# Kernel tuning notes

Hardware: AMD Instinct MI355X
Metric: run time of the kernel (lower is better)

The kernel has to match this reference:

```python
import jax, jax.numpy as jnp
import numpy as np

# dims: 64 graphs x 1024 nodes, 32768 edges/graph, 256 feats, 64 pools/graph
B, NPG, EPG, F, C = 64, 1024, 32768, 256, 64
N, E = B * NPG, B * EPG


def setup_inputs() -> dict:
    key = jax.random.key(0)
    k1, k2, k3, k4, k5 = jax.random.split(key, 5)
    x = jax.random.normal(k1, (N, F), jnp.float32)
    # within-graph edges (block structure, as in real batched graphs)
    src = jax.random.randint(k2, (B, EPG), 0, NPG, dtype=jnp.int32)
    dst = jax.random.randint(k3, (B, EPG), 0, NPG, dtype=jnp.int32)
    off = (jnp.arange(B, dtype=jnp.int32) * NPG)[:, None]
    edge_index = jnp.stack([(src + off).reshape(-1), (dst + off).reshape(-1)], 0)
    edge_weight = jax.random.uniform(k4, (E,), jnp.float32)
    batch = jnp.repeat(jnp.arange(B, dtype=jnp.int32), NPG)
    batch_ptr = jnp.arange(B + 1, dtype=jnp.int32) * NPG
    # pooling_net stand-in: linear d_feat -> num_pools
    W = jax.random.normal(k5, (F, C), jnp.float32) * 0.05
    b = jnp.zeros((C,), jnp.float32)
    return dict(x=x, edge_index=edge_index, edge_weight=edge_weight,
                batch=batch, batch_ptr=batch_ptr, W=W, b=b)


def reference(x, edge_index, edge_weight, batch, batch_ptr, W, b):
    num_batches = batch_ptr.shape[0] - 1
    Cp = W.shape[1]  # num_pools_per_graph
    logits = x @ W + b                       # pooling_net(x, edge_index)
    sm = jax.nn.softmax(logits, axis=-1)     # [N, C]
    c = jnp.argmax(sm, axis=-1)              # hard cluster per node [N]
    p = jnp.take_along_axis(sm, c[:, None], axis=-1)[:, 0]
    # straight-through nonzero value of s (==1.0 in forward value)
    v = 1.0 - jax.lax.stop_gradient(p) + p
    gcl = batch * Cp + c                     # global cluster id [N]
    K = num_batches * Cp
    # out = S^T x  -> segment reduce over nodes by global cluster
    out = jax.ops.segment_sum(v[:, None] * x, gcl, num_segments=K)  # [K, F]
    # out_adj = S^T A S  (block diagonal over graphs): per-edge scatter
    src, dst = edge_index[0], edge_index[1]
    ci, cj = c[src], c[dst]
    gb = batch[src]
    flat = gb * (Cp * Cp) + ci * Cp + cj
    contrib = edge_weight * v[src] * v[dst]
    out_adj = jax.ops.segment_sum(contrib, flat, num_segments=num_batches * Cp * Cp)
    # dense block-diagonal index set (torch returns coalesced nonzeros;
    # jit needs static shapes, so we enumerate all within-graph pool pairs)
    idx = jnp.arange(num_batches * Cp * Cp, dtype=jnp.int32)
    bb, rem = idx // (Cp * Cp), idx % (Cp * Cp)
    out_edge_index = jnp.stack([bb * Cp + rem // Cp, bb * Cp + rem % Cp], 0)
    # link_loss = ||A - S S^T||_F / E  via exact decomposition
    a2 = jnp.sum(edge_weight * edge_weight)
    ap = jnp.sum(jnp.where(gcl[src] == gcl[dst], contrib, 0.0))
    vs2 = jax.ops.segment_sum(v * v, gcl, num_segments=K)
    p2 = jnp.sum(vs2 * vs2)
    link_loss = jnp.sqrt(jnp.maximum(a2 - 2.0 * ap + p2, 0.0)) / edge_index.shape[1]
    batch_out = jnp.repeat(jnp.arange(num_batches, dtype=jnp.int32), Cp)
    batch_ptr_out = jnp.arange(num_batches + 1, dtype=jnp.int32) * Cp
    return (out, out_edge_index, out_adj, link_loss, jnp.float32(0.0),
            batch_out, batch_ptr_out)
```

## Files before the change

kernel.cpp:

```cpp
#include <hip/hip_runtime.h>
#include <cstdint>
#include <cstddef>

typedef __attribute__((ext_vector_type(8))) short short8;
typedef __attribute__((ext_vector_type(4))) float f32x4;

#define GLOAD_LDS16(gsrc, ldst) \
    __builtin_amdgcn_global_load_lds( \
        (const __attribute__((address_space(1))) void*)(gsrc), \
        (__attribute__((address_space(3))) void*)(ldst), 16, 0, 0)

namespace {
constexpr int kN    = 65536;
constexpr int kF    = 256;
constexpr int kC    = 64;
constexpr int kNPG  = 1024;
constexpr int kB    = 64;
constexpr int kE    = 2097152;
constexpr int kK    = kB * kC;

constexpr size_t OFF_OUT  = 0;
constexpr size_t OFF_EIDX = (size_t)kK * kF;
constexpr size_t OFF_ADJ  = OFF_EIDX + 2ull*kB*kC*kC;
constexpr size_t OFF_LL   = OFF_ADJ + (size_t)kB*kC*kC;
constexpr size_t OFF_Z    = OFF_LL + 1;
constexpr size_t OFF_BOUT = OFF_Z + 1;
constexpr size_t OFF_BPTR = OFF_BOUT + kK;

constexpr size_t WS_C    = 0;
constexpr size_t WS_V    = 262144;
constexpr size_t WS_VS2  = 524288;
constexpr size_t WS_A2   = 540672;
constexpr size_t WS_PERM = 544768;
constexpr size_t WS_STRT = 806912;
constexpr size_t WS_WPH  = 1048576;
constexpr size_t WS_WPL  = 1081344;
constexpr size_t WS_PADJ = 544768;

__device__ __forceinline__ unsigned short bf16_rn(float f)
{
    const unsigned int b = __float_as_uint(f);
    return (unsigned short)((b + 0x7fffu + ((b >> 16) & 1u)) >> 16);
}
}

__global__ __launch_bounds__(256) void k_const(float* __restrict__ out,
                                               const float* __restrict__ Wm,
                                               unsigned short* __restrict__ wph,
                                               unsigned short* __restrict__ wpl)
{
    const int i = blockIdx.x * 256 + threadIdx.x;
    constexpr int E2 = 2 * kB * kC * kC;
    constexpr int B3 = E2 + kK + kB + 1;
    if (i < E2) {
        const int half = i >= kB*kC*kC;
        const int idx  = half ? i - kB*kC*kC : i;
        const int bb = idx >> 12, rem = idx & 4095;
        const int val = half ? bb*kC + (rem & 63) : bb*kC + (rem >> 6);
        out[OFF_EIDX + i] = (float)val;
    } else if (i < E2 + kK) {
        const int j = i - E2;
        out[OFF_BOUT + j] = (float)(j >> 6);
    } else if (i < B3) {
        const int j = i - (E2 + kK);
        out[OFF_BPTR + j] = (float)(j * kC);
    } else if (i < B3 + 32768) {
        const int j  = (i - B3) & 16383;
        const int lo = (i - B3) >= 16384;
        const int jj = j & 7, lane = (j >> 3) & 63;
        const int nt = (j >> 9) & 3, ks = j >> 11;
        const float wv = Wm[(size_t)(ks*32 + (lane>>4)*8 + jj)*kC
                            + nt*16 + (lane & 15)];
        const unsigned short h = bf16_rn(wv);
        if (!lo) {
            wph[j] = h;
        } else {
            const float hf = __uint_as_float((unsigned int)h << 16);
            wpl[j] = bf16_rn(wv - hf);
        }
    }
}

__global__ __launch_bounds__(256) void k_logits(
    const float* __restrict__ x, const unsigned short* __restrict__ wph,
    const unsigned short* __restrict__ wpl, const float* __restrict__ bv,
    int* __restrict__ carr, float* __restrict__ varr)
{
    __shared__ unsigned short wlds[32768];
    __shared__ float xsl[2][64 * 32];
    const int tid  = threadIdx.x;
    const int lane = tid & 63;
    const int w    = tid >> 6;
    const int nbase = blockIdx.x * 64;
    const int l15  = lane & 15;
    const int kgrp = lane >> 4;

    const int snode = lane >> 3;
    const int sfo   = ((lane & 7) ^ snode) * 4;

    f32x4 acc[4];
#pragma unroll
    for (int nt = 0; nt < 4; ++nt) acc[nt] = f32x4{0.f, 0.f, 0.f, 0.f};

#pragma unroll
    for (int t = 0; t < 8; ++t) {
        GLOAD_LDS16(wph + ((size_t)t*256 + tid)*8,
                    &wlds[(t*256 + w*64)*8]);
        GLOAD_LDS16(wpl + ((size_t)t*256 + tid)*8,
                    &wlds[16384 + (t*256 + w*64)*8]);
    }
#pragma unroll
    for (int i = 0; i < 2; ++i) {
        const float* src = x + (size_t)(nbase + w*16 + i*8 + snode)*kF + sfo;
        GLOAD_LDS16(src, &xsl[0][(w*16 + i*8)*32]);
    }
    asm volatile("s_waitcnt vmcnt(0)" ::: "memory");
    __syncthreads();

#pragma unroll 1
    for (int c = 0; c < 8; ++c) {
        if (c < 7) {
#pragma unroll
            for (int i = 0; i < 2; ++i) {
                const float* src = x + (size_t)(nbase + w*16 + i*8 + snode)*kF
                                     + (c+1)*32 + sfo;
                GLOAD_LDS16(src, &xsl[(c+1) & 1][(w*16 + i*8)*32]);
            }
            asm volatile("s_waitcnt vmcnt(2)" ::: "memory");
        } else {
            asm volatile("s_waitcnt vmcnt(0)" ::: "memory");
        }

        const float* __restrict__ xb = &xsl[c & 1][0];
        short8 bh[4], bl[4];
#pragma unroll
        for (int nt = 0; nt < 4; ++nt) {
            const int wo = ((c*4 + nt)*64 + lane) * 8;
            bh[nt] = *reinterpret_cast<const short8*>(&wlds[wo]);
            bl[nt] = *reinterpret_cast<const short8*>(&wlds[16384 + wo]);
        }
        const int row = w*16 + l15;
        const int sA  = ((kgrp*2)     ^ (l15 & 7)) * 4;
        const int sC  = ((kgrp*2 + 1) ^ (l15 & 7)) * 4;
        const float4 xa = *reinterpret_cast<const float4*>(&xb[row*32 + sA]);
        const float4 xc = *reinterpret_cast<const float4*>(&xb[row*32 + sC]);
        const float xv[8] = {xa.x, xa.y, xa.z, xa.w,
                             xc.x, xc.y, xc.z, xc.w};
        short8 ah, al;
#pragma unroll
        for (int j = 0; j < 8; ++j) {
            const unsigned short h = bf16_rn(xv[j]);
            const float hf = __uint_as_float((unsigned int)h << 16);
            ah[j] = (short)h;
            al[j] = (short)bf16_rn(xv[j] - hf);
        }
#pragma unroll
        for (int nt = 0; nt < 4; ++nt) {
            acc[nt] = __builtin_amdgcn_mfma_f32_16x16x32_bf16(
                ah, bh[nt], acc[nt], 0, 0, 0);
            acc[nt] = __builtin_amdgcn_mfma_f32_16x16x32_bf16(
                al, bh[nt], acc[nt], 0, 0, 0);
            acc[nt] = __builtin_amdgcn_mfma_f32_16x16x32_bf16(
                ah, bl[nt], acc[nt], 0, 0, 0);
            acc[nt] = __builtin_amdgcn_mfma_f32_16x16x32_bf16(
                al, bl[nt], acc[nt], 0, 0, 0);
        }
    }

#pragma unroll
    for (int nt = 0; nt < 4; ++nt) {
        const float b = bv[nt*16 + l15];
#pragma unroll
        for (int r = 0; r < 4; ++r) acc[nt][r] += b;
    }
#pragma unroll
    for (int r = 0; r < 4; ++r) {
        float m = acc[0][r]; int ci = l15;
#pragma unroll
        for (int nt = 1; nt < 4; ++nt) {
            if (acc[nt][r] > m) { m = acc[nt][r]; ci = nt*16 + l15; }
        }
#pragma unroll
        for (int off = 1; off < 16; off <<= 1) {
            const float om = __shfl_xor(m, off);
            const int   oc = __shfl_xor(ci, off);
            if (om > m || (om == m && oc < ci)) { m = om; ci = oc; }
        }
        float s = 0.f;
#pragma unroll
        for (int nt = 0; nt < 4; ++nt) s += expf(acc[nt][r] - m);
#pragma unroll
        for (int off = 1; off < 16; off <<= 1) s += __shfl_xor(s, off);
        if (l15 == r) {
            const float p = 1.0f / s;
            const int n = nbase + w*16 + kgrp*4 + r;
            carr[n] = ci;
            varr[n] = (1.0f - p) + p;
        }
    }
}

__global__ __launch_bounds__(1024) void k_sort(
    const int* __restrict__ carr, int* __restrict__ perm,
    int* __restrict__ startc)
{
    __shared__ int hist[16][64];
    __shared__ int startS[65];
    const int g = blockIdx.x;
    const int tid = threadIdx.x;
    const int w = tid >> 6, lane = tid & 63;
    const int c = carr[g*kNPG + tid];
    hist[tid >> 6][tid & 63] = 0;
    __syncthreads();
    unsigned long long mm = ~0ull;
#pragma unroll
    for (int b = 0; b < 6; ++b) {
        const unsigned long long bal = __ballot((c >> b) & 1);
        mm &= ((c >> b) & 1) ? bal : ~bal;
    }
    const unsigned long long ltmask =
        (lane == 0) ? 0ull : (~0ull >> (64 - lane));
    const int rank_in_wave = __popcll(mm & ltmask);
    const int leader = __ffsll((unsigned long long)mm) - 1;
    if (lane == leader) hist[w][c] = __popcll(mm);
    __syncthreads();
    if (w == 0) {
        int tot = 0;
#pragma unroll
        for (int i = 0; i < 16; ++i) tot += hist[i][lane];
        int pre = tot;
#pragma unroll
        for (int off = 1; off < 64; off <<= 1) {
            const int t = __shfl_up(pre, off);
            if (lane >= off) pre += t;
        }
        startS[lane + 1] = pre;
        if (lane == 0) startS[0] = 0;
    }
    __syncthreads();
    int before = startS[c];
    for (int i = 0; i < w; ++i) before += hist[i][c];
    perm[g*kNPG + before + rank_in_wave] = g*kNPG + tid;
    if (tid < 65) startc[g*65 + tid] = startS[tid];
}

__global__ __launch_bounds__(1024) void k_pool_x(
    const float* __restrict__ x, const int* __restrict__ perm,
    const int* __restrict__ startc, const float* __restrict__ varr,
    float* __restrict__ out, float* __restrict__ vs2)
{
    const int tid  = threadIdx.x;
    const int g    = blockIdx.x >> 3;
    const int fh   = blockIdx.x & 7;
    const int w    = tid >> 6;
    const int lane = tid & 63;
    const int q    = lane & 7;
    const int sub  = lane >> 3;
    const int fbase = fh*32 + q*4;
#pragma unroll
    for (int cc = 0; cc < 4; ++cc) {
        const int c = w*4 + cc;
        const int s = startc[g*65 + c];
        const int e = startc[g*65 + c + 1];
        float ax = 0.f, ay = 0.f, az = 0.f, aw = 0.f, v2 = 0.f;
        for (int base = s + sub; base < e; base += 8) {
            const int n = perm[(size_t)g*kNPG + base];
            const float v = varr[n];
            const float4 xv = *reinterpret_cast<const float4*>(
                x + (size_t)n*kF + fbase);
            ax = fmaf(v, xv.x, ax); ay = fmaf(v, xv.y, ay);
            az = fmaf(v, xv.z, az); aw = fmaf(v, xv.w, aw);
            v2 = fmaf(v, v, v2);
        }
#pragma unroll
        for (int off = 8; off < 64; off <<= 1) {
            ax += __shfl_xor(ax, off); ay += __shfl_xor(ay, off);
            az += __shfl_xor(az, off); aw += __shfl_xor(aw, off);
            v2 += __shfl_xor(v2, off);
        }
        if (sub == 0) {
            const float4 o = {ax, ay, az, aw};
            *reinterpret_cast<float4*>(
                out + OFF_OUT + (size_t)(g*kC + c)*kF + fbase) = o;
        }
        if (fh == 0 && lane == 0) vs2[g*kC + c] = v2;
    }
}

__global__ __launch_bounds__(1024) void k_adj(
    const int* __restrict__ ei, const float* __restrict__ ew,
    const int* __restrict__ carr, const float* __restrict__ varr,
    float* __restrict__ padj, float* __restrict__ a2p)
{
    __shared__ float adj[kC*kC];
    __shared__ float vls[kNPG];
    __shared__ int   cls[kNPG];
    __shared__ float wred[16];
    const int tid = threadIdx.x;
    const int bid = blockIdx.x;
    const int g   = bid >> 3;
    for (int i = tid; i < kC*kC; i += 1024) adj[i] = 0.f;
    vls[tid] = varr[g*kNPG + tid];
    cls[tid] = carr[g*kNPG + tid];
    __syncthreads();
    const int e0 = bid * 4096;
    float a2l = 0.f;
#pragma unroll
    for (int it = 0; it < 4; ++it) {
        const int e  = e0 + it*1024 + tid;
        const int sn = ei[e]      & (kNPG - 1);
        const int dn = ei[kE + e] & (kNPG - 1);
        const float wv = ew[e];
        a2l += wv * wv;
        atomicAdd(&adj[cls[sn]*kC + cls[dn]], wv * vls[sn] * vls[dn]);
    }
    __syncthreads();
#pragma unroll
    for (int r = 0; r < 4; ++r) {
        const int lin = r*1024 + tid;
        padj[(size_t)bid*4096 + lin] = adj[lin];
    }
#pragma unroll
    for (int off = 32; off > 0; off >>= 1) a2l += __shfl_down(a2l, off);
    if ((tid & 63) == 0) wred[tid >> 6] = a2l;
    __syncthreads();
    if (tid == 0) {
        float s = 0.f;
#pragma unroll
        for (int wv = 0; wv < 16; ++wv) s += wred[wv];
        a2p[bid] = s;
    }
}

__global__ __launch_bounds__(256) void k_adj_merge(
    const float* __restrict__ padj, float* __restrict__ out)
{
    const int id = blockIdx.x*256 + threadIdx.x;
    const int g = id >> 12, idx = id & 4095;
    float s = 0.f;
#pragma unroll
    for (int sp = 0; sp < 8; ++sp) s += padj[(size_t)(g*8 + sp)*4096 + idx];
    out[OFF_ADJ + id] = s;
}

__global__ __launch_bounds__(256) void k_final(
    const float* __restrict__ vs2, const float* __restrict__ a2p,
    float* __restrict__ out)
{
    const int tid = threadIdx.x;
    float p2l = 0.f, apl = 0.f;
#pragma unroll
    for (int r = 0; r < 16; ++r) {
        const int k = r*256 + tid;
        const float t = vs2[k];
        p2l += t*t;
        const int g = k >> 6, cc = k & 63;
        apl += out[OFF_ADJ + (size_t)g*4096 + cc*65];
    }
    float a2l = a2p[tid] + a2p[tid + 256];
#pragma unroll
    for (int off = 32; off > 0; off >>= 1) {
        p2l += __shfl_down(p2l, off);
        apl += __shfl_down(apl, off);
        a2l += __shfl_down(a2l, off);
    }
    __shared__ float red[3][4];
    if ((tid & 63) == 0) {
        red[0][tid>>6] = p2l; red[1][tid>>6] = apl; red[2][tid>>6] = a2l;
    }
    __syncthreads();
    if (tid == 0) {
        const float p2 = red[0][0]+red[0][1]+red[0][2]+red[0][3];
        const float ap = red[1][0]+red[1][1]+red[1][2]+red[1][3];
        const float a2 = red[2][0]+red[2][1]+red[2][2]+red[2][3];
        const float val = a2 - 2.0f*ap + p2;
        out[OFF_LL] = sqrtf(fmaxf(val, 0.f)) / (float)kE;
        out[OFF_Z]  = 0.0f;
    }
}

extern "C" void kernel_launch(void* const* d_in, const int* in_sizes, int n_in,
                              void* d_out, int out_size, void* d_ws, size_t ws_size,
                              hipStream_t stream)
{
    const float* x  = (const float*)d_in[0];
    const int*   ei = (const int*)d_in[1];
    const float* ew = (const float*)d_in[2];
    const float* Wm = (const float*)d_in[5];
    const float* bv = (const float*)d_in[6];
    float* out = (float*)d_out;
    char*  ws  = (char*)d_ws;
    int*   carr  = (int*)(ws + WS_C);
    float* varr  = (float*)(ws + WS_V);
    float* vs2   = (float*)(ws + WS_VS2);
    float* a2p   = (float*)(ws + WS_A2);
    int*   perm  = (int*)(ws + WS_PERM);
    int*   strt  = (int*)(ws + WS_STRT);
    unsigned short* wph = (unsigned short*)(ws + WS_WPH);
    unsigned short* wpl = (unsigned short*)(ws + WS_WPL);
    float* padj  = (float*)(ws + WS_PADJ);

    k_const    <<<2193, 256, 0, stream>>>(out, Wm, wph, wpl);
    k_logits   <<<1024, 256, 0, stream>>>(x, wph, wpl, bv, carr, varr);
    k_sort     <<<64,  1024, 0, stream>>>(carr, perm, strt);
    k_pool_x   <<<512, 1024, 0, stream>>>(x, perm, strt, varr, out, vs2);
    k_adj      <<<512, 1024, 0, stream>>>(ei, ew, carr, varr, padj, a2p);
    k_adj_merge<<<1024, 256, 0, stream>>>(padj, out);
    k_final    <<<1,    256, 0, stream>>>(vs2, a2p, out);
}
```

Baseline: 76.49 us.

## Fuse sort, pooling and adjacency kernels into one launch with in-LDS permutation

Replaces the separate sort, pool_x and adj kernels with a single 1024-block kernel. The first 512 blocks each redo the per-graph counting sort into shared memory and then pool x. The other 512 blocks build the partial adjacency. This removes two launches and the global perm/start round trip, and lets pooling and adjacency blocks run concurrently. The adj_merge kernel now also reduces the diagonal sums, so the final kernel no longer gathers strided diagonal entries. The trade-off is that the sort is done 8 times per graph instead of once, and the heterogeneous blocks may balance unevenly.

After: 66.30 us. -13.3%, faster.

```diff
diff --git a/kernel.cpp b/kernel.cpp
--- a/kernel.cpp
+++ b/kernel.cpp
@@ -31,11 +31,10 @@
 constexpr size_t WS_V    = 262144;
 constexpr size_t WS_VS2  = 524288;
 constexpr size_t WS_A2   = 540672;
-constexpr size_t WS_PERM = 544768;
-constexpr size_t WS_STRT = 806912;
 constexpr size_t WS_WPH  = 1048576;
 constexpr size_t WS_WPL  = 1081344;
-constexpr size_t WS_PADJ = 544768;
+constexpr size_t WS_PADJ = 1114112;
+constexpr size_t WS_DSUM = 9502720;
 
 __device__ __forceinline__ unsigned short bf16_rn(float f)
 {
@@ -104,8 +103,7 @@
 
 #pragma unroll
     for (int t = 0; t < 8; ++t) {
-        GLOAD_LDS16(wph + ((size_t)t*256 + tid)*8,
-                    &wlds[(t*256 + w*64)*8]);
+        GLOAD_LDS16(wph + ((size_t)t*256 + tid)*8, &wlds[(t*256 + w*64)*8]);
         GLOAD_LDS16(wpl + ((size_t)t*256 + tid)*8,
                     &wlds[16384 + (t*256 + w*64)*8]);
     }
@@ -200,163 +198,164 @@
     }
 }
 
-__global__ __launch_bounds__(1024) void k_sort(
-    const int* __restrict__ carr, int* __restrict__ perm,
-    int* __restrict__ startc)
-{
-    __shared__ int hist[16][64];
-    __shared__ int startS[65];
-    const int g = blockIdx.x;
-    const int tid = threadIdx.x;
-    const int w = tid >> 6, lane = tid & 63;
-    const int c = carr[g*kNPG + tid];
-    hist[tid >> 6][tid & 63] = 0;
-    __syncthreads();
-    unsigned long long mm = ~0ull;
-#pragma unroll
-    for (int b = 0; b < 6; ++b) {
-        const unsigned long long bal = __ballot((c >> b) & 1);
-        mm &= ((c >> b) & 1) ? bal : ~bal;
-    }
-    const unsigned long long ltmask =
-        (lane == 0) ? 0ull : (~0ull >> (64 - lane));
-    const int rank_in_wave = __popcll(mm & ltmask);
-    const int leader = __ffsll((unsigned long long)mm) - 1;
-    if (lane == leader) hist[w][c] = __popcll(mm);
-    __syncthreads();
-    if (w == 0) {
-        int tot = 0;
-#pragma unroll
-        for (int i = 0; i < 16; ++i) tot += hist[i][lane];
-        int pre = tot;
-#pragma unroll
-        for (int off = 1; off < 64; off <<= 1) {
-            const int t = __shfl_up(pre, off);
-            if (lane >= off) pre += t;
-        }
-        startS[lane + 1] = pre;
-        if (lane == 0) startS[0] = 0;
-    }
-    __syncthreads();
-    int before = startS[c];
-    for (int i = 0; i < w; ++i) before += hist[i][c];
-    perm[g*kNPG + before + rank_in_wave] = g*kNPG + tid;
-    if (tid < 65) startc[g*65 + tid] = startS[tid];
-}
-
-__global__ __launch_bounds__(1024) void k_pool_x(
-    const float* __restrict__ x, const int* __restrict__ perm,
-    const int* __restrict__ startc, const float* __restrict__ varr,
-    float* __restrict__ out, float* __restrict__ vs2)
-{
-    const int tid  = threadIdx.x;
-    const int g    = blockIdx.x >> 3;
-    const int fh   = blockIdx.x & 7;
-    const int w    = tid >> 6;
-    const int lane = tid & 63;
-    const int q    = lane & 7;
-    const int sub  = lane >> 3;
-    const int fbase = fh*32 + q*4;
-#pragma unroll
-    for (int cc = 0; cc < 4; ++cc) {
-        const int c = w*4 + cc;
-        const int s = startc[g*65 + c];
-        const int e = startc[g*65 + c + 1];
-        float ax = 0.f, ay = 0.f, az = 0.f, aw = 0.f, v2 = 0.f;
-        for (int base = s + sub; base < e; base += 8) {
-            const int n = perm[(size_t)g*kNPG + base];
-            const float v = varr[n];
-            const float4 xv = *reinterpret_cast<const float4*>(
-                x + (size_t)n*kF + fbase);
-            ax = fmaf(v, xv.x, ax); ay = fmaf(v, xv.y, ay);
-            az = fmaf(v, xv.z, az); aw = fmaf(v, xv.w, aw);
-            v2 = fmaf(v, v, v2);
-        }
-#pragma unroll
-        for (int off = 8; off < 64; off <<= 1) {
-            ax += __shfl_xor(ax, off); ay += __shfl_xor(ay, off);
-            az += __shfl_xor(az, off); aw += __shfl_xor(aw, off);
-            v2 += __shfl_xor(v2, off);
-        }
-        if (sub == 0) {
-            const float4 o = {ax, ay, az, aw};
-            *reinterpret_cast<float4*>(
-                out + OFF_OUT + (size_t)(g*kC + c)*kF + fbase) = o;
-        }
-        if (fh == 0 && lane == 0) vs2[g*kC + c] = v2;
-    }
-}
-
-__global__ __launch_bounds__(1024) void k_adj(
-    const int* __restrict__ ei, const float* __restrict__ ew,
-    const int* __restrict__ carr, const float* __restrict__ varr,
-    float* __restrict__ padj, float* __restrict__ a2p)
-{
-    __shared__ float adj[kC*kC];
-    __shared__ float vls[kNPG];
-    __shared__ int   cls[kNPG];
-    __shared__ float wred[16];
+__global__ __launch_bounds__(1024) void k_fused(
+    const float* __restrict__ x, const int* __restrict__ carr,
+    const float* __restrict__ varr, const int* __restrict__ ei,
+    const float* __restrict__ ew, float* __restrict__ out,
+    float* __restrict__ vs2, float* __restrict__ padj,
+    float* __restrict__ a2p)
+{
+    __shared__ char smem[25152];
     const int tid = threadIdx.x;
     const int bid = blockIdx.x;
-    const int g   = bid >> 3;
-    for (int i = tid; i < kC*kC; i += 1024) adj[i] = 0.f;
-    vls[tid] = varr[g*kNPG + tid];
-    cls[tid] = carr[g*kNPG + tid];
-    __syncthreads();
-    const int e0 = bid * 4096;
-    float a2l = 0.f;
-#pragma unroll
-    for (int it = 0; it < 4; ++it) {
-        const int e  = e0 + it*1024 + tid;
-        const int sn = ei[e]      & (kNPG - 1);
-        const int dn = ei[kE + e] & (kNPG - 1);
-        const float wv = ew[e];
-        a2l += wv * wv;
-        atomicAdd(&adj[cls[sn]*kC + cls[dn]], wv * vls[sn] * vls[dn]);
-    }
-    __syncthreads();
-#pragma unroll
-    for (int r = 0; r < 4; ++r) {
-        const int lin = r*1024 + tid;
-        padj[(size_t)bid*4096 + lin] = adj[lin];
-    }
-#pragma unroll
-    for (int off = 32; off > 0; off >>= 1) a2l += __shfl_down(a2l, off);
-    if ((tid & 63) == 0) wred[tid >> 6] = a2l;
-    __syncthreads();
-    if (tid == 0) {
-        float s = 0.f;
-#pragma unroll
-        for (int wv = 0; wv < 16; ++wv) s += wred[wv];
-        a2p[bid] = s;
+
+    if (bid < 512) {
+        int* hist   = (int*)smem;
+        int* startS = hist + 1024;
+        int* permL  = startS + 80;
+        const int g  = bid >> 3;
+        const int fh = bid & 7;
+        const int w = tid >> 6, lane = tid & 63;
+
+        const int c = carr[g*kNPG + tid];
+        hist[tid] = 0;
+        __syncthreads();
+        unsigned long long mm = ~0ull;
+#pragma unroll
+        for (int b = 0; b < 6; ++b) {
+            const unsigned long long bal = __ballot((c >> b) & 1);
+            mm &= ((c >> b) & 1) ? bal : ~bal;
+        }
+        const unsigned long long ltmask =
+            (lane == 0) ? 0ull : (~0ull >> (64 - lane));
+        const int rank_in_wave = __popcll(mm & ltmask);
+        const int leader = __ffsll((unsigned long long)mm) - 1;
+        if (lane == leader) hist[w*64 + c] = __popcll(mm);
+        __syncthreads();
+        if (w == 0) {
+            int tot = 0;
+#pragma unroll
+            for (int i = 0; i < 16; ++i) tot += hist[i*64 + lane];
+            int pre = tot;
+#pragma unroll
+            for (int off = 1; off < 64; off <<= 1) {
+                const int t = __shfl_up(pre, off);
+                if (lane >= off) pre += t;
+            }
+            startS[lane + 1] = pre;
+            if (lane == 0) startS[0] = 0;
+        }
+        __syncthreads();
+        int before = startS[c];
+        for (int i = 0; i < w; ++i) before += hist[i*64 + c];
+        permL[before + rank_in_wave] = tid;
+        __syncthreads();
+
+        const int q   = lane & 7;
+        const int sub = lane >> 3;
+        const int fbase = fh*32 + q*4;
+#pragma unroll
+        for (int cc = 0; cc < 4; ++cc) {
+            const int cl = w*4 + cc;
+            const int s = startS[cl];
+            const int e = startS[cl + 1];
+            float ax = 0.f, ay = 0.f, az = 0.f, aw = 0.f, v2 = 0.f;
+            for (int base = s + sub; base < e; base += 8) {
+                const int n = g*kNPG + permL[base];
+                const float v = varr[n];
+                const float4 xv = *reinterpret_cast<const float4*>(
+                    x + (size_t)n*kF + fbase);
+                ax = fmaf(v, xv.x, ax); ay = fmaf(v, xv.y, ay);
+                az = fmaf(v, xv.z, az); aw = fmaf(v, xv.w, aw);
+                v2 = fmaf(v, v, v2);
+            }
+#pragma unroll
+            for (int off = 8; off < 64; off <<= 1) {
+                ax += __shfl_xor(ax, off); ay += __shfl_xor(ay, off);
+                az += __shfl_xor(az, off); aw += __shfl_xor(aw, off);
+                v2 += __shfl_xor(v2, off);
+            }
+            if (sub == 0) {
+                const float4 o = {ax, ay, az, aw};
+                *reinterpret_cast<float4*>(
+                    out + OFF_OUT + (size_t)(g*kC + cl)*kF + fbase) = o;
+            }
+            if (fh == 0 && lane == 0) vs2[g*kC + cl] = v2;
+        }
+    } else {
+        float* adj = (float*)smem;
+        float* vls = adj + 4096;
+        int*   cls = (int*)(vls + 1024);
+        float* wred = (float*)(cls + 1024);
+        const int bid2 = bid - 512;
+        const int g = bid2 >> 3;
+        for (int i = tid; i < kC*kC; i += 1024) adj[i] = 0.f;
+        vls[tid] = varr[g*kNPG + tid];
+        cls[tid] = carr[g*kNPG + tid];
+        __syncthreads();
+        const int e0 = bid2 * 4096;
+        float a2l = 0.f;
+#pragma unroll
+        for (int it = 0; it < 4; ++it) {
+            const int e  = e0 + it*1024 + tid;
+            const int sn = ei[e]      & (kNPG - 1);
+            const int dn = ei[kE + e] & (kNPG - 1);
+            const float wv = ew[e];
+            a2l += wv * wv;
+            atomicAdd(&adj[cls[sn]*kC + cls[dn]], wv * vls[sn] * vls[dn]);
+        }
+        __syncthreads();
+#pragma unroll
+        for (int r = 0; r < 4; ++r) {
+            const int lin = r*1024 + tid;
+            padj[(size_t)bid2*4096 + lin] = adj[lin];
+        }
+#pragma unroll
+        for (int off = 32; off > 0; off >>= 1) a2l += __shfl_down(a2l, off);
+        if ((tid & 63) == 0) wred[tid >> 6] = a2l;
+        __syncthreads();
+        if (tid == 0) {
+            float s = 0.f;
+#pragma unroll
+            for (int wv = 0; wv < 16; ++wv) s += wred[wv];
+            a2p[bid2] = s;
+        }
     }
 }
 
 __global__ __launch_bounds__(256) void k_adj_merge(
-    const float* __restrict__ padj, float* __restrict__ out)
-{
-    const int id = blockIdx.x*256 + threadIdx.x;
+    const float* __restrict__ padj, float* __restrict__ out,
+    float* __restrict__ dsum)
+{
+    __shared__ float red[4];
+    const int tid = threadIdx.x;
+    const int id = blockIdx.x*256 + tid;
     const int g = id >> 12, idx = id & 4095;
     float s = 0.f;
 #pragma unroll
     for (int sp = 0; sp < 8; ++sp) s += padj[(size_t)(g*8 + sp)*4096 + idx];
     out[OFF_ADJ + id] = s;
+    float d = ((idx % 65) == 0) ? s : 0.f;
+#pragma unroll
+    for (int off = 32; off > 0; off >>= 1) d += __shfl_down(d, off);
+    if ((tid & 63) == 0) red[tid >> 6] = d;
+    __syncthreads();
+    if (tid == 0) dsum[blockIdx.x] = red[0] + red[1] + red[2] + red[3];
 }
 
 __global__ __launch_bounds__(256) void k_final(
     const float* __restrict__ vs2, const float* __restrict__ a2p,
-    float* __restrict__ out)
+    const float* __restrict__ dsum, float* __restrict__ out)
 {
     const int tid = threadIdx.x;
     float p2l = 0.f, apl = 0.f;
 #pragma unroll
     for (int r = 0; r < 16; ++r) {
-        const int k = r*256 + tid;
-        const float t = vs2[k];
+        const float t = vs2[r*256 + tid];
         p2l += t*t;
-        const int g = k >> 6, cc = k & 63;
-        apl += out[OFF_ADJ + (size_t)g*4096 + cc*65];
-    }
+    }
+#pragma unroll
+    for (int r = 0; r < 4; ++r) apl += dsum[r*256 + tid];
     float a2l = a2p[tid] + a2p[tid + 256];
 #pragma unroll
     for (int off = 32; off > 0; off >>= 1) {
@@ -394,17 +393,15 @@
     float* varr  = (float*)(ws + WS_V);
     float* vs2   = (float*)(ws + WS_VS2);
     float* a2p   = (float*)(ws + WS_A2);
-    int*   perm  = (int*)(ws + WS_PERM);
-    int*   strt  = (int*)(ws + WS_STRT);
     unsigned short* wph = (unsigned short*)(ws + WS_WPH);
     unsigned short* wpl = (unsigned short*)(ws + WS_WPL);
     float* padj  = (float*)(ws + WS_PADJ);
+    float* dsum  = (float*)(ws + WS_DSUM);
 
     k_const    <<<2193, 256, 0, stream>>>(out, Wm, wph, wpl);
     k_logits   <<<1024, 256, 0, stream>>>(x, wph, wpl, bv, carr, varr);
-    k_sort     <<<64,  1024, 0, stream>>>(carr, perm, strt);
-    k_pool_x   <<<512, 1024, 0, stream>>>(x, perm, strt, varr, out, vs2);
-    k_adj      <<<512, 1024, 0, stream>>>(ei, ew, carr, varr, padj, a2p);
-    k_adj_merge<<<1024, 256, 0, stream>>>(padj, out);
-    k_final    <<<1,    256, 0, stream>>>(vs2, a2p, out);
-}
+    k_fused    <<<1024, 1024, 0, stream>>>(x, carr, varr, ei, ew,
+                                           out, vs2, padj, a2p);
+    k_adj_merge<<<1024, 256, 0, stream>>>(padj, out, dsum);
+    k_final    <<<1,    256, 0, stream>>>(vs2, a2p, dsum, out);
+}
```
